# Kernel optimization log

Measured on AMD Instinct MI355X. Metric: run time of the kernel, lower is better.

Reference implementation:

```python
import jax, jax.numpy as jnp
import numpy as np
from jax import lax

N = 500_000          # num voxels
LATENT = 128         # latent_dim
DESC = 32            # descriptor_dim
G = 128              # voxel grid side
B = 2                # batches
K = 256              # max centers (hardcoded topk in module)
TAU = 0.1
MIN_SCORE = 0.5
R = 1                # peak_radius
BASE = G + 2         # padded hash base so stencil offsets never collide
NEG = -1e30

# radius_graph with r = R + 0.1 on integer coords -> exact stencil offsets
_OFFS = [(dx, dy, dz)
         for dx in range(-R, R + 1)
         for dy in range(-R, R + 1)
         for dz in range(-R, R + 1)
         if dx * dx + dy * dy + dz * dz <= (R + 0.1) ** 2]
DKEYS = np.array([dx * BASE * BASE + dy * BASE + dz for dx, dy, dz in _OFFS], np.int32)  # (7,)


def setup_inputs() -> dict:
    rng = np.random.default_rng(0)
    lin = rng.choice(B * G ** 3, size=N, replace=False)  # unique occupied voxels
    b = lin // G ** 3
    rem = lin % G ** 3
    coords = np.stack([b, rem // (G * G), (rem // G) % G, rem % G], 1).astype(np.int32)
    key = jax.random.key(0)
    k1, k2, k3, k4, k5, k6, k7 = jax.random.split(key, 7)
    s = 1.0 / np.sqrt(LATENT)
    return {
        "coords": jnp.asarray(coords),
        "voxel_feats": jax.random.normal(k1, (N, LATENT), jnp.float32),
        "centroid_scores": jax.random.uniform(k2, (N, 1), jnp.float32),
        "Wv": jax.random.normal(k3, (LATENT, DESC), jnp.float32) * s,
        "bv": jax.random.normal(k4, (DESC,), jnp.float32) * 0.01,
        "Wc": jax.random.normal(k5, (LATENT, DESC), jnp.float32) * s,
        "bc": jax.random.normal(k6, (DESC,), jnp.float32) * 0.01,
        "bg": jax.random.normal(k7, (DESC,), jnp.float32) * 0.02,
    }


def _find_centroid_peaks(coords, voxel_feats, centroid_scores):
    """Replicates _find_centroid_peaks with fixed K=256 padding (torch.no_grad block)."""
    n = coords.shape[0]
    scores = centroid_scores[:, 0]
    mask = scores > TAU
    # hash each voxel; +1 padding so stencil neighbors never wrap across rows/batches
    keyv = (coords[:, 0] * BASE + coords[:, 1] + 1) * BASE * BASE \
         + (coords[:, 2] + 1) * BASE + (coords[:, 3] + 1)
    order = jnp.argsort(keyv)
    keys_s = keyv[order]
    ms = jnp.where(mask, scores, NEG)  # only masked points participate in the graph

    nk = keyv[:, None] + jnp.asarray(DKEYS)[None, :]          # (N,7) neighbor keys
    pos = jnp.clip(jnp.searchsorted(keys_s, nk.ravel()), 0, n - 1).reshape(n, len(DKEYS))
    found = keys_s[pos] == nk                                  # (N,7) geometric hit
    j = order[pos]                                             # (N,7) neighbor index
    found = found & mask[j] & mask[:, None]                    # edges need both masked

    neigh_max = jnp.max(jnp.where(found, ms[j], NEG), axis=1)  # scatter_max over edges
    peak_mask = mask & (scores >= neigh_max - 1e-6) & (scores >= MIN_SCORE)

    # topk-256 peaks (padded with NEG if fewer)
    vals, top_idx = lax.top_k(jnp.where(peak_mask, scores, NEG), K)
    valid_peak = vals > NEG / 2
    owner_init = jnp.full((n,), -1, jnp.int32).at[top_idx].set(
        jnp.where(valid_peak, jnp.arange(K, dtype=jnp.int32), -1))

    # ownership propagation: a voxel is owned by a neighboring (top) peak; self-loop
    # keeps peaks owning themselves. Conflicts resolved by max (torch scatter is
    # nondeterministic here).
    owner = jnp.max(jnp.where(found, owner_init[j], -1), axis=1)
    owner = jnp.where(mask, owner, -1)

    valid = owner >= 0
    owner_safe = jnp.where(valid, owner, 0)
    sums = jax.ops.segment_sum(jnp.where(valid[:, None], voxel_feats, 0.0),
                               owner_safe, num_segments=K)
    counts = jax.ops.segment_sum(valid.astype(jnp.float32), owner_safe, num_segments=K)
    feat_mean = sums / jnp.maximum(counts, 1.0)[:, None]       # scatter_mean
    conf = jnp.where(valid_peak, vals, 0.0)[:, None]           # (K,1)
    return conf, feat_mean


def reference(coords, voxel_feats, centroid_scores, Wv, bv, Wc, bc, bg):
    conf, feat_mean = _find_centroid_peaks(coords, voxel_feats, centroid_scores)
    conf = lax.stop_gradient(conf)
    feat_mean = lax.stop_gradient(feat_mean)
    voxel_desc = voxel_feats @ Wv + bv              # 1x1 sparse conv == linear
    center_desc = feat_mean @ Wc + bc               # 1x1 sparse conv == linear
    cols = jnp.concatenate([bg[None, :], conf * center_desc], axis=0)  # (K+1, DESC)
    instance_output = voxel_desc @ cols.T            # (N, K+1)
    return conf, instance_output
```

## Files before the change

### kernel.cpp

```cpp
#include <hip/hip_runtime.h>
#include <stdint.h>

#define TAUF 0.1f
#define MIN_SCOREF 0.5f
#define KTOP 256
#define BASE 130
#define BASE2 16900
#define TABLE_N 4394000
#define NEGF (-1e30f)
#define CAP2 3072
#define NSMAX 4096
#define ROWS_PB 192
#define CHUNK 32

__global__ void k_build(const int* __restrict__ coords, int* __restrict__ table,
                        int* __restrict__ keys, int n) {
  int i = blockIdx.x * 256 + threadIdx.x;
  if (i >= n) return;
  int4 c = ((const int4*)coords)[i];
  int key = (c.x * BASE + c.y + 1) * BASE2 + (c.z + 1) * BASE + (c.w + 1);
  keys[i] = key;
  table[key] = i;
}

__global__ void k_peak(const float* __restrict__ scores, const int* __restrict__ keys,
                       const int* __restrict__ table, uint2* __restrict__ cand,
                       int* __restrict__ cand_cnt, int* __restrict__ hist, int n) {
  int i = blockIdx.x * 256 + threadIdx.x;
  if (i >= n) return;
  float s = scores[i];
  if (!(s > TAUF)) return;
  int key = keys[i];
  const int dk[7] = {-BASE2, -BASE, -1, 0, 1, BASE, BASE2};
  float nm = NEGF;
#pragma unroll
  for (int o = 0; o < 7; ++o) {
    int j = table[key + dk[o]];
    if (j >= 0) {
      float sj = scores[j];
      if (sj > TAUF) nm = fmaxf(nm, sj);
    }
  }
  if (s >= nm - 1e-6f && s >= MIN_SCOREF) {
    int p = atomicAdd(cand_cnt, 1);
    if (p < n) cand[p] = make_uint2(__float_as_uint(s), (unsigned)i);
    unsigned sb = __float_as_uint(s);
    int b = (int)((sb - 0x3F000000u) >> 12);
    b = min(max(b, 0), 2047);
    atomicAdd(&hist[b], 1);
  }
}

__global__ __launch_bounds__(1024) void k_select(const uint2* __restrict__ cand,
                                                 const int* __restrict__ cand_cnt,
                                                 const int* __restrict__ hist,
                                                 float* __restrict__ conf_out,
                                                 int* __restrict__ owner_init,
                                                 int* __restrict__ peak_vox) {
  __shared__ int hist_s[2048];
  __shared__ int part[64];
  __shared__ unsigned long long keys_s[NSMAX];
  __shared__ int bstar_s, m_s;
  int t = threadIdx.x;
  int nc = *cand_cnt;
  for (int b = t; b < 2048; b += 1024) hist_s[b] = hist[b];
  if (t == 0) m_s = 0;
  __syncthreads();
  if (t < 64) {
    int acc = 0;
    for (int b = t * 32; b < t * 32 + 32; ++b) acc += hist_s[b];
    part[t] = acc;
  }
  __syncthreads();
  if (t == 0) {
    int target = min(nc, KTOP);
    int bs = 0;
    if (target > 0) {
      int run = 0, w = 63;
      for (; w >= 0; --w) {
        if (run + part[w] >= target) break;
        run += part[w];
      }
      if (w < 0) {
        bs = 0;
      } else {
        for (int b = w * 32 + 31;; --b) {
          run += hist_s[b];
          if (run >= target || b == w * 32) { bs = b; break; }
        }
      }
    }
    bstar_s = bs;
  }
  __syncthreads();
  int bs = bstar_s;
  for (int idx = t; idx < nc; idx += 1024) {
    uint2 cv = cand[idx];
    int b = (int)((cv.x - 0x3F000000u) >> 12);
    b = min(max(b, 0), 2047);
    if (b >= bs) {
      int p = atomicAdd(&m_s, 1);
      if (p < CAP2)
        keys_s[p] = ((unsigned long long)cv.x << 32) | (unsigned)(~cv.y);
    }
  }
  __syncthreads();
  int m = min(m_s, CAP2);
  int ns = 256;
  while (ns < m) ns <<= 1;
  for (int idx = t; idx < ns; idx += 1024)
    if (idx >= m) keys_s[idx] = 0ULL;
  __syncthreads();
  for (int k2 = 2; k2 <= ns; k2 <<= 1) {
    for (int j2 = k2 >> 1; j2 > 0; j2 >>= 1) {
      for (int i = t; i < ns; i += 1024) {
        int ixj = i ^ j2;
        if (ixj > i) {
          unsigned long long a = keys_s[i], b = keys_s[ixj];
          bool descSeg = ((i & k2) == 0);
          bool sw = descSeg ? (a < b) : (a > b);
          if (sw) { keys_s[i] = b; keys_s[ixj] = a; }
        }
      }
      __syncthreads();
    }
  }
  if (t < KTOP) {
    int navail = min(nc, KTOP);
    if (t < navail) {
      unsigned long long kk = keys_s[t];
      float sc = __uint_as_float((unsigned)(kk >> 32));
      int vi = (int)(~(unsigned)(kk & 0xFFFFFFFFu));
      conf_out[t] = sc;
      owner_init[vi] = t;
      peak_vox[t] = vi;
    } else {
      conf_out[t] = 0.0f;
      peak_vox[t] = -1;
    }
  }
}

__global__ void k_owner(const float* __restrict__ scores, const int* __restrict__ keys,
                        const int* __restrict__ table, const int* __restrict__ owner_init,
                        const int* __restrict__ peak_vox, int* __restrict__ visited,
                        const float* __restrict__ feats, float* __restrict__ sums,
                        float* __restrict__ counts) {
  int t = blockIdx.x * blockDim.x + threadIdx.x;
  if (t >= KTOP * 7) return;
  int p = t / 7, o = t % 7;
  int v0 = peak_vox[p];
  if (v0 < 0) return;
  const int dk[7] = {-BASE2, -BASE, -1, 0, 1, BASE, BASE2};
  int v = table[keys[v0] + dk[o]];
  if (v < 0) return;
  if (!(scores[v] > TAUF)) return;
  int kv = keys[v];
  int own = -1;
#pragma unroll
  for (int oo = 0; oo < 7; ++oo) {
    int j = table[kv + dk[oo]];
    if (j >= 0 && scores[j] > TAUF) own = max(own, owner_init[j]);
  }
  if (own < 0) return;
  if (atomicCAS(&visited[v], 0, 1) == 0) {
    atomicAdd(&counts[own], 1.0f);
    const float* fv = feats + (size_t)v * 128;
    float* so = sums + own * 128;
    for (int d = 0; d < 128; ++d) atomicAdd(&so[d], fv[d]);
  }
}

__global__ void k_cols(const float* __restrict__ sums, const float* __restrict__ counts,
                       const float* __restrict__ conf, const float* __restrict__ Wc,
                       const float* __restrict__ bc, const float* __restrict__ bg,
                       float* __restrict__ colsT) {
  int gid = blockIdx.x * blockDim.x + threadIdx.x;
  if (gid >= 32 * 257) return;
  int kd = gid / 257, jo = gid % 257;
  float val;
  if (jo == 0) {
    val = bg[kd];
  } else {
    int p = jo - 1;
    float inv = 1.0f / fmaxf(counts[p], 1.0f);
    float acc = bc[kd];
    const float* sp = sums + p * 128;
    for (int c = 0; c < 128; ++c) acc += sp[c] * inv * Wc[c * 32 + kd];
    val = conf[p] * acc;
  }
  colsT[kd * 257 + jo] = val;
}

__global__ __launch_bounds__(256) void k_go(const float* __restrict__ feats,
                                            const float* __restrict__ Wv,
                                            const float* __restrict__ bv,
                                            const float* __restrict__ colsT,
                                            float* __restrict__ out, int n) {
  __shared__ __align__(16) float Wv_s[128 * 32];
  __shared__ __align__(16) float cols_s[32 * 260];
  __shared__ __align__(16) float feats_s[CHUNK * 129];
  __shared__ float desc_s[CHUNK * 33];
  __shared__ float bv_s[32];
  int t = threadIdx.x;
  int rbase = blockIdx.x * ROWS_PB;
  {
    const float4* src = (const float4*)Wv;
    float4* dst = (float4*)Wv_s;
    for (int i = t; i < 1024; i += 256) dst[i] = src[i];
  }
  for (int idx = t; idx < 32 * 257; idx += 256) {
    int kd = idx / 257, jo = idx % 257;
    cols_s[kd * 260 + jo] = colsT[idx];
  }
  if (t < 32) bv_s[t] = bv[t];

  for (int c0 = 0; c0 < ROWS_PB; c0 += CHUNK) {
    __syncthreads();
    {
      int idx = t;
      for (int it = 0; it < 4; ++it, idx += 256) {
        int r = idx >> 5, q = idx & 31;
        int row = rbase + c0 + r;
        float4 v = make_float4(0.f, 0.f, 0.f, 0.f);
        if (row < n) v = *(const float4*)(feats + (size_t)row * 128 + q * 4);
        float* fd = &feats_s[r * 129 + q * 4];
        fd[0] = v.x; fd[1] = v.y; fd[2] = v.z; fd[3] = v.w;
      }
    }
    __syncthreads();
    {
      int r = t & 31, k0 = (t >> 5) * 4;
      float a0 = bv_s[k0], a1 = bv_s[k0 + 1], a2 = bv_s[k0 + 2], a3 = bv_s[k0 + 3];
      const float* fr = &feats_s[r * 129];
#pragma unroll 8
      for (int c = 0; c < 128; ++c) {
        float f = fr[c];
        float4 w = *(const float4*)&Wv_s[c * 32 + k0];
        a0 += f * w.x; a1 += f * w.y; a2 += f * w.z; a3 += f * w.w;
      }
      float* dd = &desc_s[r * 33 + k0];
      dd[0] = a0; dd[1] = a1; dd[2] = a2; dd[3] = a3;
    }
    __syncthreads();
    {
      int rg = t >> 3, jg = t & 7;
      int row = rbase + c0 + rg;
      if (row < n) {
        float dreg[32];
#pragma unroll
        for (int k = 0; k < 32; ++k) dreg[k] = desc_s[rg * 33 + k];
        float* op = out + 256 + (size_t)row * 257;
        for (int jc = 0; jc < 4; ++jc) {
          int j0 = jc * 64 + jg * 8;
          float acc[8];
#pragma unroll
          for (int j = 0; j < 8; ++j) acc[j] = 0.f;
#pragma unroll 4
          for (int k = 0; k < 32; ++k) {
            float f = dreg[k];
            float4 cA = *(const float4*)&cols_s[k * 260 + j0];
            float4 cB = *(const float4*)&cols_s[k * 260 + j0 + 4];
            acc[0] += f * cA.x; acc[1] += f * cA.y; acc[2] += f * cA.z; acc[3] += f * cA.w;
            acc[4] += f * cB.x; acc[5] += f * cB.y; acc[6] += f * cB.z; acc[7] += f * cB.w;
          }
#pragma unroll
          for (int j = 0; j < 8; ++j) op[j0 + j] = acc[j];
        }
        if (jg == 0) {
          float accT = 0.f;
#pragma unroll 8
          for (int k = 0; k < 32; ++k) accT += dreg[k] * cols_s[k * 260 + 256];
          op[256] = accT;
        }
      }
    }
  }
}

extern "C" void kernel_launch(void* const* d_in, const int* in_sizes, int n_in,
                              void* d_out, int out_size, void* d_ws, size_t ws_size,
                              hipStream_t stream) {
  const int*   coords = (const int*)d_in[0];
  const float* feats  = (const float*)d_in[1];
  const float* scores = (const float*)d_in[2];
  const float* Wv     = (const float*)d_in[3];
  const float* bv     = (const float*)d_in[4];
  const float* Wc     = (const float*)d_in[5];
  const float* bc     = (const float*)d_in[6];
  const float* bg     = (const float*)d_in[7];
  float* out = (float*)d_out;
  int n = in_sizes[0] / 4;

  char* ws = (char*)d_ws;
  size_t off = 0;
  auto alloc = [&](size_t bytes) -> char* {
    char* p = ws + off;
    off = (off + bytes + 255) & ~(size_t)255;
    return p;
  };
  int*   table      = (int*)alloc((size_t)TABLE_N * 4);
  int*   owner_init = (int*)alloc((size_t)n * 4);
  size_t ff_bytes   = off;
  int*   keys       = (int*)alloc((size_t)n * 4);
  char*  zero_base  = ws + off;
  int*   visited    = (int*)alloc((size_t)n * 4);
  int*   cand_cnt   = (int*)alloc(256);
  int*   hist       = (int*)alloc(2048 * 4);
  float* sums       = (float*)alloc(256 * 128 * 4);
  float* counts     = (float*)alloc(256 * 4);
  size_t zero_bytes = (size_t)((ws + off) - zero_base);
  uint2* cand       = (uint2*)alloc((size_t)n * 8);
  int*   peak_vox   = (int*)alloc(KTOP * 4);
  float* colsT      = (float*)alloc(32 * 257 * 4);
  (void)ws_size;

  hipMemsetAsync(table, 0xFF, ff_bytes, stream);
  hipMemsetAsync(zero_base, 0, zero_bytes, stream);

  int nb = (n + 255) / 256;
  k_build<<<nb, 256, 0, stream>>>(coords, table, keys, n);
  k_peak<<<nb, 256, 0, stream>>>(scores, keys, table, cand, cand_cnt, hist, n);
  k_select<<<1, 1024, 0, stream>>>(cand, cand_cnt, hist, out, owner_init, peak_vox);
  k_owner<<<7, 256, 0, stream>>>(scores, keys, table, owner_init, peak_vox,
                                 visited, feats, sums, counts);
  k_cols<<<(32 * 257 + 255) / 256, 256, 0, stream>>>(sums, counts, out, Wc, bc, bg, colsT);
  k_go<<<(n + ROWS_PB - 1) / ROWS_PB, 256, 0, stream>>>(feats, Wv, bv, colsT, out, n);
}
```

Measured before the change: 1.174 ms.

## Compute each output row in one thread, dropping staged shared-memory tiles

```diff
diff --git a/kernel.cpp b/kernel.cpp
--- a/kernel.cpp
+++ b/kernel.cpp
@@ -10,8 +10,6 @@
 #define NEGF (-1e30f)
 #define CAP2 3072
 #define NSMAX 4096
-#define ROWS_PB 192
-#define CHUNK 32
 
 __global__ void k_build(const int* __restrict__ coords, int* __restrict__ table,
                         int* __restrict__ keys, int n) {
@@ -192,18 +190,15 @@
   colsT[kd * 257 + jo] = val;
 }
 
-__global__ __launch_bounds__(256) void k_go(const float* __restrict__ feats,
-                                            const float* __restrict__ Wv,
-                                            const float* __restrict__ bv,
-                                            const float* __restrict__ colsT,
-                                            float* __restrict__ out, int n) {
+__global__ __launch_bounds__(256) void k_rows(const float* __restrict__ feats,
+                                              const float* __restrict__ Wv,
+                                              const float* __restrict__ bv,
+                                              const float* __restrict__ colsT,
+                                              float* __restrict__ out, int n) {
   __shared__ __align__(16) float Wv_s[128 * 32];
   __shared__ __align__(16) float cols_s[32 * 260];
-  __shared__ __align__(16) float feats_s[CHUNK * 129];
-  __shared__ float desc_s[CHUNK * 33];
   __shared__ float bv_s[32];
   int t = threadIdx.x;
-  int rbase = blockIdx.x * ROWS_PB;
   {
     const float4* src = (const float4*)Wv;
     float4* dst = (float4*)Wv_s;
@@ -214,67 +209,66 @@
     cols_s[kd * 260 + jo] = colsT[idx];
   }
   if (t < 32) bv_s[t] = bv[t];
-
-  for (int c0 = 0; c0 < ROWS_PB; c0 += CHUNK) {
-    __syncthreads();
-    {
-      int idx = t;
-      for (int it = 0; it < 4; ++it, idx += 256) {
-        int r = idx >> 5, q = idx & 31;
-        int row = rbase + c0 + r;
-        float4 v = make_float4(0.f, 0.f, 0.f, 0.f);
-        if (row < n) v = *(const float4*)(feats + (size_t)row * 128 + q * 4);
-        float* fd = &feats_s[r * 129 + q * 4];
-        fd[0] = v.x; fd[1] = v.y; fd[2] = v.z; fd[3] = v.w;
-      }
-    }
-    __syncthreads();
-    {
-      int r = t & 31, k0 = (t >> 5) * 4;
-      float a0 = bv_s[k0], a1 = bv_s[k0 + 1], a2 = bv_s[k0 + 2], a3 = bv_s[k0 + 3];
-      const float* fr = &feats_s[r * 129];
-#pragma unroll 8
-      for (int c = 0; c < 128; ++c) {
-        float f = fr[c];
-        float4 w = *(const float4*)&Wv_s[c * 32 + k0];
-        a0 += f * w.x; a1 += f * w.y; a2 += f * w.z; a3 += f * w.w;
-      }
-      float* dd = &desc_s[r * 33 + k0];
-      dd[0] = a0; dd[1] = a1; dd[2] = a2; dd[3] = a3;
-    }
-    __syncthreads();
-    {
-      int rg = t >> 3, jg = t & 7;
-      int row = rbase + c0 + rg;
-      if (row < n) {
-        float dreg[32];
-#pragma unroll
-        for (int k = 0; k < 32; ++k) dreg[k] = desc_s[rg * 33 + k];
-        float* op = out + 256 + (size_t)row * 257;
-        for (int jc = 0; jc < 4; ++jc) {
-          int j0 = jc * 64 + jg * 8;
-          float acc[8];
-#pragma unroll
-          for (int j = 0; j < 8; ++j) acc[j] = 0.f;
-#pragma unroll 4
-          for (int k = 0; k < 32; ++k) {
-            float f = dreg[k];
-            float4 cA = *(const float4*)&cols_s[k * 260 + j0];
-            float4 cB = *(const float4*)&cols_s[k * 260 + j0 + 4];
-            acc[0] += f * cA.x; acc[1] += f * cA.y; acc[2] += f * cA.z; acc[3] += f * cA.w;
-            acc[4] += f * cB.x; acc[5] += f * cB.y; acc[6] += f * cB.z; acc[7] += f * cB.w;
-          }
-#pragma unroll
-          for (int j = 0; j < 8; ++j) op[j0 + j] = acc[j];
-        }
-        if (jg == 0) {
-          float accT = 0.f;
-#pragma unroll 8
-          for (int k = 0; k < 32; ++k) accT += dreg[k] * cols_s[k * 260 + 256];
-          op[256] = accT;
-        }
-      }
-    }
+  __syncthreads();
+
+  int row = blockIdx.x * 256 + t;
+  if (row >= n) return;
+
+  float d[32];
+#pragma unroll
+  for (int k = 0; k < 32; ++k) d[k] = bv_s[k];
+  const float* fr = feats + (size_t)row * 128;
+  for (int c0 = 0; c0 < 128; c0 += 16) {
+    float4 f0 = *(const float4*)(fr + c0);
+    float4 f1 = *(const float4*)(fr + c0 + 4);
+    float4 f2 = *(const float4*)(fr + c0 + 8);
+    float4 f3 = *(const float4*)(fr + c0 + 12);
+    float fs[16] = {f0.x, f0.y, f0.z, f0.w, f1.x, f1.y, f1.z, f1.w,
+                    f2.x, f2.y, f2.z, f2.w, f3.x, f3.y, f3.z, f3.w};
+#pragma unroll
+    for (int cc = 0; cc < 16; ++cc) {
+      float f = fs[cc];
+      const float* wr = &Wv_s[(c0 + cc) * 32];
+      float4 w0 = *(const float4*)(wr + 0);
+      float4 w1 = *(const float4*)(wr + 4);
+      float4 w2 = *(const float4*)(wr + 8);
+      float4 w3 = *(const float4*)(wr + 12);
+      float4 w4 = *(const float4*)(wr + 16);
+      float4 w5 = *(const float4*)(wr + 20);
+      float4 w6 = *(const float4*)(wr + 24);
+      float4 w7 = *(const float4*)(wr + 28);
+      d[0] += f * w0.x; d[1] += f * w0.y; d[2] += f * w0.z; d[3] += f * w0.w;
+      d[4] += f * w1.x; d[5] += f * w1.y; d[6] += f * w1.z; d[7] += f * w1.w;
+      d[8] += f * w2.x; d[9] += f * w2.y; d[10] += f * w2.z; d[11] += f * w2.w;
+      d[12] += f * w3.x; d[13] += f * w3.y; d[14] += f * w3.z; d[15] += f * w3.w;
+      d[16] += f * w4.x; d[17] += f * w4.y; d[18] += f * w4.z; d[19] += f * w4.w;
+      d[20] += f * w5.x; d[21] += f * w5.y; d[22] += f * w5.z; d[23] += f * w5.w;
+      d[24] += f * w6.x; d[25] += f * w6.y; d[26] += f * w6.z; d[27] += f * w6.w;
+      d[28] += f * w7.x; d[29] += f * w7.y; d[30] += f * w7.z; d[31] += f * w7.w;
+    }
+  }
+
+  float* op = out + 256 + (size_t)row * 257;
+  for (int j0 = 0; j0 < 256; j0 += 8) {
+    float acc[8];
+#pragma unroll
+    for (int j = 0; j < 8; ++j) acc[j] = 0.f;
+#pragma unroll
+    for (int k = 0; k < 32; ++k) {
+      float f = d[k];
+      float4 cA = *(const float4*)&cols_s[k * 260 + j0];
+      float4 cB = *(const float4*)&cols_s[k * 260 + j0 + 4];
+      acc[0] += f * cA.x; acc[1] += f * cA.y; acc[2] += f * cA.z; acc[3] += f * cA.w;
+      acc[4] += f * cB.x; acc[5] += f * cB.y; acc[6] += f * cB.z; acc[7] += f * cB.w;
+    }
+#pragma unroll
+    for (int j = 0; j < 8; ++j) op[j0 + j] = acc[j];
+  }
+  {
+    float accT = 0.f;
+#pragma unroll
+    for (int k = 0; k < 32; ++k) accT += d[k] * cols_s[k * 260 + 256];
+    op[256] = accT;
   }
 }
 
@@ -325,5 +319,5 @@
   k_owner<<<7, 256, 0, stream>>>(scores, keys, table, owner_init, peak_vox,
                                  visited, feats, sums, counts);
   k_cols<<<(32 * 257 + 255) / 256, 256, 0, stream>>>(sums, counts, out, Wc, bc, bg, colsT);
-  k_go<<<(n + ROWS_PB - 1) / ROWS_PB, 256, 0, stream>>>(feats, Wv, bv, colsT, out, n);
-}
+  k_rows<<<nb, 256, 0, stream>>>(feats, Wv, bv, colsT, out, n);
+}
```

Result: faster. 1.126 ms (-4.1%).
